# Performance work log

Measured on AMD Instinct MI355X. Metric: run time of the kernel, lower is better.

Reference implementation:

```python
import jax, jax.numpy as jnp
import numpy as np

# LLaMA-style decoder config (shrunken for reference): L layers, hidden D, H heads,
# SwiGLU width F, vocab V, LoRA rank R.
B, S, D, H, F, V, L, R = 2, 512, 1024, 16, 4096, 32000, 2, 16
DH = D // H
LORA_ALPHA = 32.0
EPS = 1e-5
ROPE_THETA = 10000.0


def setup_inputs() -> dict:
    key = jax.random.key(0)
    ks = iter(jax.random.split(key, 40))
    def n(shape, std=0.02):
        return jax.random.normal(next(ks), shape, jnp.float32) * std
    return {
        "input_ids": jax.random.randint(next(ks), (B, S), 0, V),
        "attention_mask": jnp.ones((B, S), jnp.int32),
        "embed": n((V, D)),
        "ln1": jnp.ones((L, D), jnp.float32),
        "ln2": jnp.ones((L, D), jnp.float32),
        "wq": n((L, D, D)), "aq": n((L, D, R)), "bq": n((L, R, D), 0.01),
        "wk": n((L, D, D)), "ak": n((L, D, R)), "bk": n((L, R, D), 0.01),
        "wv": n((L, D, D)), "av": n((L, D, R)), "bv": n((L, R, D), 0.01),
        "wo": n((L, D, D)), "ao": n((L, D, R)), "bo": n((L, R, D), 0.01),
        "wg": n((L, D, F)), "ag": n((L, D, R)), "bg": n((L, R, F), 0.01),
        "wu": n((L, D, F)), "au": n((L, D, R)), "bu": n((L, R, F), 0.01),
        "wd": n((L, F, D)), "ad": n((L, F, R)), "bd": n((L, R, D), 0.01),
        "final_ln": jnp.ones((D,), jnp.float32),
        "lm_head_w": n((D, V)),
        "value_w": n((D, 1)),
        "value_b": jnp.zeros((1,), jnp.float32),
    }


def _rmsnorm(x, w):
    return x * jax.lax.rsqrt(jnp.mean(x * x, axis=-1, keepdims=True) + EPS) * w


def _lin_lora(x, w, a, b):
    # base matmul + low-rank LoRA update scaled by alpha/r (dropout=eval/off)
    return x @ w + ((x @ a) @ b) * (LORA_ALPHA / R)


def _rope_cache(seq_len):
    half = DH // 2
    inv = 1.0 / (ROPE_THETA ** (jnp.arange(half, dtype=jnp.float32) / half))
    ang = jnp.arange(seq_len, dtype=jnp.float32)[:, None] * inv  # [S, half]
    ang = jnp.concatenate([ang, ang], axis=-1)                   # [S, DH]
    return jnp.cos(ang), jnp.sin(ang)


def _apply_rope(x, cos, sin):  # x: [B,S,H,DH]
    h = DH // 2
    rot = jnp.concatenate([-x[..., h:], x[..., :h]], axis=-1)
    return x * cos[None, :, None, :] + rot * sin[None, :, None, :]


def reference(input_ids, attention_mask, embed, ln1, ln2,
              wq, aq, bq, wk, ak, bk, wv, av, bv, wo, ao, bo,
              wg, ag, bg, wu, au, bu, wd, ad, bd,
              final_ln, lm_head_w, value_w, value_b):
    h = embed[input_ids]  # [B,S,D]
    cos, sin = _rope_cache(S)
    causal = jnp.tril(jnp.ones((S, S), bool))
    keep = causal[None, None, :, :] & (attention_mask[:, None, None, :] > 0)
    bias = jnp.where(keep, 0.0, -1e9)  # [B,1,S,S]
    scale = 1.0 / jnp.sqrt(jnp.float32(DH))

    for i in range(L):
        # --- self-attention block ---
        x = _rmsnorm(h, ln1[i])
        q = _lin_lora(x, wq[i], aq[i], bq[i]).reshape(B, S, H, DH)
        k = _lin_lora(x, wk[i], ak[i], bk[i]).reshape(B, S, H, DH)
        v = _lin_lora(x, wv[i], av[i], bv[i]).reshape(B, S, H, DH)
        q = _apply_rope(q, cos, sin)
        k = _apply_rope(k, cos, sin)
        scores = jnp.einsum("bqhd,bkhd->bhqk", q, k) * scale + bias
        attn = jax.nn.softmax(scores, axis=-1)
        o = jnp.einsum("bhqk,bkhd->bqhd", attn, v).reshape(B, S, D)
        h = h + _lin_lora(o, wo[i], ao[i], bo[i])
        # --- SwiGLU MLP block ---
        x = _rmsnorm(h, ln2[i])
        g = jax.nn.silu(_lin_lora(x, wg[i], ag[i], bg[i]))
        u = _lin_lora(x, wu[i], au[i], bu[i])
        h = h + _lin_lora(g * u, wd[i], ad[i], bd[i])

    h = _rmsnorm(h, final_ln)          # HF hidden_states[-1] is post final norm
    logits = h @ lm_head_w             # [B,S,V]
    values = (h @ value_w)[..., 0] + value_b[0]  # [B,S] (squeeze(-1))
    return logits, values
```

## Files before the change

kernel.cpp:

```cpp
#include <hip/hip_runtime.h>
#include <math.h>

constexpr int B = 2, S = 512, D = 1024, H = 16, F = 4096, V = 32000, L = 2, R = 16, DH = 64;
constexpr int BS = B * S;
constexpr float LORA_SCALE = 2.0f;
constexpr float EPS = 1e-5f;
constexpr int RS_QKV = 3 * D;
constexpr int RS_GU  = 2 * F;

typedef __attribute__((ext_vector_type(8))) __bf16 bf16x8;
typedef __attribute__((ext_vector_type(4))) float f32x4;

__device__ __forceinline__ unsigned short f2bf(float f) {
  unsigned u = __builtin_bit_cast(unsigned, f);
  unsigned r = (u + 0x7FFFu + ((u >> 16) & 1u)) >> 16;
  return (unsigned short)r;
}
__device__ __forceinline__ float bf2f(unsigned short us) {
  return __builtin_bit_cast(float, (unsigned)us << 16);
}
__device__ __forceinline__ void load_lds16(const void* g, void* l) {
  __builtin_amdgcn_global_load_lds((const __attribute__((address_space(1))) void*)g,
                                   (__attribute__((address_space(3))) void*)l, 16, 0, 0);
}

struct Ptr3 { const float* p[3]; };

__global__ void rope_cache_kernel(float* __restrict__ cosb, float* __restrict__ sinb) {
  int s = blockIdx.x, j = threadIdx.x;
  float inv = __expf(-(float)j * (9.210340371976184f / 32.0f));
  float ang = (float)s * inv;
  float c = cosf(ang), sn = sinf(ang);
  cosb[s * DH + j] = c;  cosb[s * DH + j + 32] = c;
  sinb[s * DH + j] = sn; sinb[s * DH + j + 32] = sn;
}

__global__ void embed_kernel(const int* __restrict__ ids, const float* __restrict__ emb,
                             float* __restrict__ h) {
  int row = blockIdx.x, t = threadIdx.x;
  int id = ids[row];
  ((float4*)(h + (size_t)row * D))[t] = ((const float4*)(emb + (size_t)id * D))[t];
}

__global__ void rmsnorm_bf16_kernel(const float* __restrict__ x, const float* __restrict__ w,
                                    unsigned short* __restrict__ y) {
  int row = blockIdx.x, t = threadIdx.x;
  float4 xv = ((const float4*)(x + (size_t)row * D))[t];
  float ss = xv.x * xv.x + xv.y * xv.y + xv.z * xv.z + xv.w * xv.w;
  __shared__ float red[256];
  red[t] = ss; __syncthreads();
  for (int s2 = 128; s2; s2 >>= 1) { if (t < s2) red[t] += red[t + s2]; __syncthreads(); }
  float rinv = rsqrtf(red[0] * (1.0f / D) + EPS);
  float4 wv = ((const float4*)w)[t];
  ushort4 o;
  o.x = f2bf(xv.x * rinv * wv.x); o.y = f2bf(xv.y * rinv * wv.y);
  o.z = f2bf(xv.z * rinv * wv.z); o.w = f2bf(xv.w * rinv * wv.w);
  ((ushort4*)(y + (size_t)row * D))[t] = o;
}

template <int NA>
__global__ void rms_lora_kernel(const float* __restrict__ hp, const float* __restrict__ w,
                                Ptr3 ap, unsigned short* __restrict__ xbf,
                                unsigned short* __restrict__ t2e) {
  int row = blockIdx.x, t = threadIdx.x;
  int lane = t & 63;
  __shared__ float xs[D];
  __shared__ float red[256];
  float4 xv = ((const float4*)(hp + (size_t)row * D))[t];
  float ss = xv.x * xv.x + xv.y * xv.y + xv.z * xv.z + xv.w * xv.w;
  red[t] = ss; __syncthreads();
  for (int s2 = 128; s2; s2 >>= 1) { if (t < s2) red[t] += red[t + s2]; __syncthreads(); }
  float rinv = rsqrtf(red[0] * (1.0f / D) + EPS);
  float4 wv = ((const float4*)w)[t];
  float4 nx;
  nx.x = xv.x * rinv * wv.x; nx.y = xv.y * rinv * wv.y;
  nx.z = xv.z * rinv * wv.z; nx.w = xv.w * rinv * wv.w;
  xs[t * 4 + 0] = nx.x; xs[t * 4 + 1] = nx.y; xs[t * 4 + 2] = nx.z; xs[t * 4 + 3] = nx.w;
  ushort4 o;
  o.x = f2bf(nx.x); o.y = f2bf(nx.y); o.z = f2bf(nx.z); o.w = f2bf(nx.w);
  ((ushort4*)(xbf + (size_t)row * D))[t] = o;
  if (t >= NA * 16 && t < 64) t2e[(size_t)row * 64 + t] = 0;
  __syncthreads();
  int n = t & 15, g = t >> 4;
#pragma unroll
  for (int ad = 0; ad < NA; ++ad) {
    const float* a = ap.p[ad];
    float s = 0.0f;
    for (int k = g; k < D; k += 16) s = fmaf(xs[k], a[k * 16 + n], s);
    s += __shfl_xor(s, 16);
    s += __shfl_xor(s, 32);
    if (lane < 16) red[(t >> 6) * 16 + n] = s;
    __syncthreads();
    if (t < 16) t2e[(size_t)row * 64 + ad * 16 + t] =
        f2bf(LORA_SCALE * (red[t] + red[t + 16] + red[t + 32] + red[t + 48]));
    if (ad + 1 < NA) __syncthreads();
  }
}

__global__ void lora_o_kernel(const unsigned short* __restrict__ xb, const float* __restrict__ a,
                              unsigned short* __restrict__ t2e) {
  int row = blockIdx.x, t = threadIdx.x;
  int lane = t & 63;
  __shared__ float xs[D];
  __shared__ float red[64];
  for (int k = t; k < D; k += 256) xs[k] = bf2f(xb[(size_t)row * D + k]);
  if (t >= 16 && t < 64) t2e[(size_t)row * 64 + t] = 0;
  __syncthreads();
  int n = t & 15, g = t >> 4;
  float s = 0.0f;
  for (int k = g; k < D; k += 16) s = fmaf(xs[k], a[k * 16 + n], s);
  s += __shfl_xor(s, 16);
  s += __shfl_xor(s, 32);
  if (lane < 16) red[(t >> 6) * 16 + n] = s;
  __syncthreads();
  if (t < 16) t2e[(size_t)row * 64 + t] =
      f2bf(LORA_SCALE * (red[t] + red[t + 16] + red[t + 32] + red[t + 48]));
}

__global__ void silu_lora_kernel(const unsigned short* __restrict__ gub, const float* __restrict__ a,
                                 unsigned short* __restrict__ gbf, unsigned short* __restrict__ t2e) {
  int row = blockIdx.x, t = threadIdx.x;
  int lane = t & 63;
  __shared__ float xs[F];
  __shared__ float red[64];
#pragma unroll
  for (int i2 = 0; i2 < 2; ++i2) {
    int idx = i2 * 256 + t;
    uint4 gv = ((const uint4*)(gub + (size_t)row * RS_GU))[idx];
    uint4 uv = ((const uint4*)(gub + (size_t)row * RS_GU + F))[idx];
    const unsigned* gw = (const unsigned*)&gv;
    const unsigned* uw = (const unsigned*)&uv;
    unsigned short go[8];
#pragma unroll
    for (int q = 0; q < 4; ++q) {
      float g0 = bf2f((unsigned short)(gw[q] & 0xffff)), g1 = bf2f((unsigned short)(gw[q] >> 16));
      float u0 = bf2f((unsigned short)(uw[q] & 0xffff)), u1 = bf2f((unsigned short)(uw[q] >> 16));
      float r0 = g0 / (1.0f + __expf(-g0)) * u0;
      float r1 = g1 / (1.0f + __expf(-g1)) * u1;
      xs[idx * 8 + q * 2] = r0; xs[idx * 8 + q * 2 + 1] = r1;
      go[q * 2] = f2bf(r0); go[q * 2 + 1] = f2bf(r1);
    }
    *(uint4*)(gbf + (size_t)row * F + idx * 8) = *(const uint4*)go;
  }
  if (t >= 16 && t < 64) t2e[(size_t)row * 64 + t] = 0;
  __syncthreads();
  int n = t & 15, g = t >> 4;
  float s = 0.0f;
  for (int k = g; k < F; k += 16) s = fmaf(xs[k], a[k * 16 + n], s);
  s += __shfl_xor(s, 16);
  s += __shfl_xor(s, 32);
  if (lane < 16) red[(t >> 6) * 16 + n] = s;
  __syncthreads();
  if (t < 16) t2e[(size_t)row * 64 + t] =
      f2bf(LORA_SCALE * (red[t] + red[t + 16] + red[t + 32] + red[t + 48]));
}

struct BD { const float* p0; const float* p1; const float* p2;
            unsigned short* dst; int NA; int logW; int nelem; };
struct BDs { BD d[8]; };
__global__ void bext_many_kernel(BDs da) {
  int gid = blockIdx.x * 256 + threadIdx.x;
  int di = 0;
  while (gid >= da.d[di].nelem) { gid -= da.d[di].nelem; ++di; }
  const BD dd = da.d[di];
  int n = gid >> 6, kk = gid & 63;
  int W = 1 << dd.logW;
  int sel = n >> dd.logW;
  const float* bp = (sel == 0) ? dd.p0 : (sel == 1) ? dd.p1 : dd.p2;
  float v = 0.0f;
  if ((kk >> 4) == sel && sel < dd.NA)
    v = bp[(size_t)(kk & 15) * W + (n & (W - 1))];
  dd.dst[(size_t)n * 64 + kk] = f2bf(v);
}

struct TD { const float* src; unsigned short* dst; int K; int N; int nblk; };
struct TDs { TD d[15]; };
__global__ __launch_bounds__(256) void transpose_many_kernel(TDs da) {
  __shared__ unsigned short tile[64 * 136];
  int bid = blockIdx.x;
  int di = 0;
  while (bid >= da.d[di].nblk) { bid -= da.d[di].nblk; ++di; }
  const TD dd = da.d[di];
  int nbx = dd.N >> 6;
  int n0 = (bid % nbx) * 64, k0 = (bid / nbx) * 128;
  int t = threadIdx.x;
  int rr = t >> 4, c4 = (t & 15) << 2;
#pragma unroll
  for (int i = 0; i < 8; ++i) {
    int row = i * 16 + rr;
    float4 v = *(const float4*)(dd.src + (size_t)(k0 + row) * dd.N + n0 + c4);
    tile[(c4 + 0) * 136 + (row ^ ((((c4 + 0) >> 2) & 7) << 2))] = f2bf(v.x);
    tile[(c4 + 1) * 136 + (row ^ ((((c4 + 1) >> 2) & 7) << 2))] = f2bf(v.y);
    tile[(c4 + 2) * 136 + (row ^ ((((c4 + 2) >> 2) & 7) << 2))] = f2bf(v.z);
    tile[(c4 + 3) * 136 + (row ^ ((((c4 + 3) >> 2) & 7) << 2))] = f2bf(v.w);
  }
  __syncthreads();
#pragma unroll
  for (int i = 0; i < 8; ++i) {
    int flat = i * 256 + t;
    int n = flat >> 5, cw = flat & 31;
    int kb = (cw * 4) ^ (((n >> 2) & 7) << 2);
    *(ushort4*)(dd.dst + (size_t)(n0 + n) * dd.K + k0 + cw * 4) =
        *(const ushort4*)(tile + n * 136 + kb);
  }
}

template <int BN, bool ACC, bool EXT, int OM>
__global__ __launch_bounds__(256) void gemm_bf16_kernel(
    const unsigned short* __restrict__ A, const unsigned short* __restrict__ Bt,
    void* __restrict__ Cp, int M, int N, int K,
    const unsigned short* __restrict__ Ae, const unsigned short* __restrict__ Be,
    const float* __restrict__ cosb, const float* __restrict__ sinb) {
  constexpr int WM = (BN == 128) ? 2 : 4;
  constexpr int RW = 128 / WM;
  constexpr int MI = RW / 16;
  constexpr int BCH = BN / 32;
  __shared__ __align__(16) unsigned short As[2][128 * 64];
  __shared__ __align__(16) unsigned short Bs[2][BN * 64];
  int t = threadIdx.x;
  int lane = t & 63, wave = t >> 6;
  int wr = (BN == 128) ? (wave >> 1) : wave;
  int wc = (BN == 128) ? (wave & 1) : 0;
  int MT = gridDim.y, NT = gridDim.x;
  int nwg = MT * NT;
  int orig = blockIdx.y * NT + blockIdx.x;
  int qq = nwg >> 3, rr8 = nwg & 7;
  int xcd = orig & 7, pos = orig >> 3;
  int wg = (xcd < rr8) ? (xcd * (qq + 1) + pos) : (rr8 * (qq + 1) + (xcd - rr8) * qq + pos);
  int m0 = (wg % MT) * 128, n0 = (wg / MT) * BN;
  int fr = lane & 15, fq = lane >> 4;
  int xorv = fr & 7;
  f32x4 acc[MI][4] = {};
  int kIters = K / 64;
  int nIters = EXT ? kIters + 1 : kIters;

  auto STAGE = [&](int it, int buf) {
    bool ext = EXT && (it == kIters);
    int k0 = it * 64;
#pragma unroll
    for (int c = 0; c < 4; ++c) {
      int i = c * 256 + t;
      int row = i >> 3, c8 = i & 7;
      int sc = (c8 ^ (row & 7)) * 8;
      const unsigned short* src = ext ? (Ae + (size_t)(m0 + row) * 64 + sc)
                                      : (A + (size_t)(m0 + row) * K + k0 + sc);
      load_lds16(src, &As[buf][i * 8]);
    }
#pragma unroll
    for (int c = 0; c < BCH; ++c) {
      int i = c * 256 + t;
      int row = i >> 3, c8 = i & 7;
      int sc = (c8 ^ (row & 7)) * 8;
      const unsigned short* src = ext ? (Be + (size_t)(n0 + row) * 64 + sc)
                                      : (Bt + (size_t)(n0 + row) * K + k0 + sc);
      load_lds16(src, &Bs[buf][i * 8]);
    }
  };

  STAGE(0, 0);
  if (nIters > 1) STAGE(1, 1);
  int cur = 0;
  for (int it = 0; it < nIters; ++it) {
    if (it + 1 < nIters) {
      if constexpr (BN == 128) asm volatile("s_waitcnt vmcnt(8)" ::: "memory");
      else                     asm volatile("s_waitcnt vmcnt(6)" ::: "memory");
    } else {
      asm volatile("s_waitcnt vmcnt(0)" ::: "memory");
    }
    __builtin_amdgcn_s_barrier();
    __builtin_amdgcn_s_setprio(1);
#pragma unroll
    for (int kk = 0; kk < 2; ++kk) {
      bf16x8 af[MI], bfr[4];
#pragma unroll
      for (int mi = 0; mi < MI; ++mi)
        af[mi] = *(const bf16x8*)(&As[cur][(wr * RW + mi * 16 + fr) * 64 + (((kk * 4 + fq) ^ xorv) << 3)]);
#pragma unroll
      for (int ni = 0; ni < 4; ++ni)
        bfr[ni] = *(const bf16x8*)(&Bs[cur][(wc * 64 + ni * 16 + fr) * 64 + (((kk * 4 + fq) ^ xorv) << 3)]);
#pragma unroll
      for (int mi = 0; mi < MI; ++mi)
#pragma unroll
        for (int ni = 0; ni < 4; ++ni)
          acc[mi][ni] = __builtin_amdgcn_mfma_f32_16x16x32_bf16(af[mi], bfr[ni], acc[mi][ni], 0, 0, 0);
    }
    __builtin_amdgcn_s_setprio(0);
    __builtin_amdgcn_s_barrier();
    if (it + 2 < nIters) STAGE(it + 2, cur);
    cur ^= 1;
  }
  if constexpr (OM == 0) {
    float* C = (float*)Cp;
#pragma unroll
    for (int mi = 0; mi < MI; ++mi)
#pragma unroll
      for (int ni = 0; ni < 4; ++ni)
#pragma unroll
        for (int j = 0; j < 4; ++j) {
          int r = m0 + wr * RW + mi * 16 + fq * 4 + j;
          int cl = n0 + wc * 64 + ni * 16 + fr;
          size_t idx = (size_t)r * N + cl;
          float v = acc[mi][ni][j];
          C[idx] = ACC ? C[idx] + v : v;
        }
  } else {
    unsigned short* Cb = (unsigned short*)Cp;
#pragma unroll
    for (int mi = 0; mi < MI; ++mi)
#pragma unroll
      for (int j = 0; j < 4; ++j) {
        int r = m0 + wr * RW + mi * 16 + fq * 4 + j;
        if constexpr (OM == 2) {
          int s = r & (S - 1);
#pragma unroll
          for (int ni = 0; ni < 2; ++ni) {
            int cl0 = n0 + wc * 64 + ni * 16 + fr;
            int cl1 = cl0 + 32;
            float x0 = acc[mi][ni][j], x1 = acc[mi][ni + 2][j];
            if (cl0 < 2 * D) {
              int dh = cl0 & 63;
              float cz = cosb[s * DH + dh], sz = sinb[s * DH + dh];
              float y0 = x0 * cz - x1 * sz;
              float y1 = x1 * cz + x0 * sz;
              x0 = y0; x1 = y1;
            }
            Cb[(size_t)r * N + cl0] = f2bf(x0);
            Cb[(size_t)r * N + cl1] = f2bf(x1);
          }
        } else {
#pragma unroll
          for (int ni = 0; ni < 4; ++ni) {
            int cl = n0 + wc * 64 + ni * 16 + fr;
            Cb[(size_t)r * N + cl] = f2bf(acc[mi][ni][j]);
          }
        }
      }
  }
}

__global__ __launch_bounds__(128) void attn_mfma_kernel(
    const unsigned short* __restrict__ qkvb, const int* __restrict__ amask,
    unsigned short* __restrict__ o) {
  __shared__ unsigned short Qs[32 * 72];
  __shared__ unsigned short Ks[64 * 72];
  __shared__ unsigned short Vt[64 * 72];
  __shared__ unsigned short Ps[2][16 * 72];
  __shared__ float msk[64];
  int bid = blockIdx.x;
  int qt = bid & 15, hh = (bid >> 4) & (H - 1), b = bid >> 8;
  int t = threadIdx.x;
  int lane = t & 63, w = t >> 6;
  int fr = lane & 15, fq = lane >> 4;
  size_t rowbase = (size_t)b * S;
  int q0 = qt * 32;
  const float scale = 0.125f;
#pragma unroll
  for (int c = 0; c < 2; ++c) {
    int i = c * 128 + t;
    int row = i >> 3, ch = i & 7;
    *(uint4*)(Qs + row * 72 + ch * 8) =
        *(const uint4*)(qkvb + (rowbase + q0 + row) * RS_QKV + hh * DH + ch * 8);
  }
  f32x4 oacc[4] = {};
  float m_old[4] = {-1e30f, -1e30f, -1e30f, -1e30f};
  float l[4] = {};
  int qbase = q0 + w * 16;
  int nkt = ((q0 + 31) >> 6) + 1;
  for (int kt = 0; kt < nkt; ++kt) {
    int kk0 = kt * 64;
#pragma unroll
    for (int c = 0; c < 4; ++c) {
      int i = c * 128 + t;
      int row = i >> 3, ch = i & 7;
      uint4 kv = *(const uint4*)(qkvb + (rowbase + kk0 + row) * RS_QKV + D + hh * DH + ch * 8);
      *(uint4*)(Ks + row * 72 + ch * 8) = kv;
      uint4 vv = *(const uint4*)(qkvb + (rowbase + kk0 + row) * RS_QKV + 2 * D + hh * DH + ch * 8);
      const unsigned short* vs = (const unsigned short*)&vv;
#pragma unroll
      for (int q = 0; q < 8; ++q) Vt[(ch * 8 + q) * 72 + row] = vs[q];
    }
    if (t < 64) msk[t] = (amask[b * S + kk0 + t] > 0) ? 0.0f : -1e9f;
    __syncthreads();
    bf16x8 aq[2];
    aq[0] = *(const bf16x8*)(Qs + (w * 16 + fr) * 72 + fq * 8);
    aq[1] = *(const bf16x8*)(Qs + (w * 16 + fr) * 72 + 32 + fq * 8);
    f32x4 sacc[4];
    __builtin_amdgcn_s_setprio(1);
#pragma unroll
    for (int ct = 0; ct < 4; ++ct) {
      bf16x8 bk0 = *(const bf16x8*)(Ks + (ct * 16 + fr) * 72 + fq * 8);
      bf16x8 bk1 = *(const bf16x8*)(Ks + (ct * 16 + fr) * 72 + 32 + fq * 8);
      f32x4 z = {};
      z = __builtin_amdgcn_mfma_f32_16x16x32_bf16(aq[0], bk0, z, 0, 0, 0);
      sacc[ct] = __builtin_amdgcn_mfma_f32_16x16x32_bf16(aq[1], bk1, z, 0, 0, 0);
    }
    __builtin_amdgcn_s_setprio(0);
    float sv[4][4];
#pragma unroll
    for (int ct = 0; ct < 4; ++ct) {
      int kg = kk0 + ct * 16 + fr;
      float mk = msk[ct * 16 + fr];
#pragma unroll
      for (int j = 0; j < 4; ++j) {
        int qg = qbase + fq * 4 + j;
        float s = sacc[ct][j] * scale + mk;
        sv[ct][j] = (kg > qg) ? -1e9f : s;
      }
    }
    float mnew[4], f[4], rsum[4];
#pragma unroll
    for (int j = 0; j < 4; ++j) {
      float mt = fmaxf(fmaxf(sv[0][j], sv[1][j]), fmaxf(sv[2][j], sv[3][j]));
      for (int off = 1; off < 16; off <<= 1) mt = fmaxf(mt, __shfl_xor(mt, off));
      mnew[j] = fmaxf(m_old[j], mt);
      f[j] = __expf(m_old[j] - mnew[j]);
      float rs = 0.0f;
#pragma unroll
      for (int ct = 0; ct < 4; ++ct) {
        float e = __expf(sv[ct][j] - mnew[j]);
        sv[ct][j] = e;
        rs += e;
      }
      for (int off = 1; off < 16; off <<= 1) rs += __shfl_xor(rs, off);
      rsum[j] = rs;
      l[j] = l[j] * f[j] + rsum[j];
      m_old[j] = mnew[j];
#pragma unroll
      for (int dt = 0; dt < 4; ++dt) oacc[dt][j] *= f[j];
    }
#pragma unroll
    for (int ct = 0; ct < 4; ++ct)
#pragma unroll
      for (int j = 0; j < 4; ++j)
        Ps[w][(fq * 4 + j) * 72 + ct * 16 + fr] = f2bf(sv[ct][j]);
    __syncthreads();
    bf16x8 pa[2];
    pa[0] = *(const bf16x8*)(&Ps[w][fr * 72 + fq * 8]);
    pa[1] = *(const bf16x8*)(&Ps[w][fr * 72 + 32 + fq * 8]);
    __builtin_amdgcn_s_setprio(1);
#pragma unroll
    for (int dt = 0; dt < 4; ++dt) {
      bf16x8 vb0 = *(const bf16x8*)(Vt + (dt * 16 + fr) * 72 + fq * 8);
      bf16x8 vb1 = *(const bf16x8*)(Vt + (dt * 16 + fr) * 72 + 32 + fq * 8);
      oacc[dt] = __builtin_amdgcn_mfma_f32_16x16x32_bf16(pa[0], vb0, oacc[dt], 0, 0, 0);
      oacc[dt] = __builtin_amdgcn_mfma_f32_16x16x32_bf16(pa[1], vb1, oacc[dt], 0, 0, 0);
    }
    __builtin_amdgcn_s_setprio(0);
    __syncthreads();
  }
#pragma unroll
  for (int j = 0; j < 4; ++j) {
    float rinv = 1.0f / l[j];
    int qrow = qbase + fq * 4 + j;
#pragma unroll
    for (int dt = 0; dt < 4; ++dt)
      o[(rowbase + qrow) * D + hh * DH + dt * 16 + fr] = f2bf(oacc[dt][j] * rinv);
  }
}

__global__ void value_kernel(const unsigned short* __restrict__ hf, const float* __restrict__ vw,
                             const float* __restrict__ vb, float* __restrict__ out) {
  int row = blockIdx.x, t = threadIdx.x;
  float acc = 0.0f;
  for (int d = t; d < D; d += 256) acc = fmaf(bf2f(hf[(size_t)row * D + d]), vw[d], acc);
  __shared__ float red[256];
  red[t] = acc; __syncthreads();
  for (int s2 = 128; s2; s2 >>= 1) { if (t < s2) red[t] += red[t + s2]; __syncthreads(); }
  if (t == 0) out[row] = red[0] + vb[0];
}

extern "C" void kernel_launch(void* const* d_in, const int* in_sizes, int n_in,
                              void* d_out, int out_size, void* d_ws, size_t ws_size,
                              hipStream_t stream) {
  const int*   ids     = (const int*)d_in[0];
  const int*   amask   = (const int*)d_in[1];
  const float* emb     = (const float*)d_in[2];
  const float* ln1     = (const float*)d_in[3];
  const float* ln2     = (const float*)d_in[4];
  const float* wq = (const float*)d_in[5],  *aq = (const float*)d_in[6],  *bq = (const float*)d_in[7];
  const float* wk = (const float*)d_in[8],  *ak = (const float*)d_in[9],  *bk = (const float*)d_in[10];
  const float* wv = (const float*)d_in[11], *av = (const float*)d_in[12], *bv = (const float*)d_in[13];
  const float* wo = (const float*)d_in[14], *ao = (const float*)d_in[15], *bo = (const float*)d_in[16];
  const float* wg = (const float*)d_in[17], *ag = (const float*)d_in[18], *bg = (const float*)d_in[19];
  const float* wu = (const float*)d_in[20], *au = (const float*)d_in[21], *bu = (const float*)d_in[22];
  const float* wd = (const float*)d_in[23], *ad = (const float*)d_in[24], *bd = (const float*)d_in[25];
  const float* final_ln  = (const float*)d_in[26];
  const float* lm_head_w = (const float*)d_in[27];
  const float* value_w   = (const float*)d_in[28];
  const float* value_b   = (const float*)d_in[29];

  float* out    = (float*)d_out;
  float* logits = out;
  float* values = out + (size_t)BS * V;

  float* Wf = (float*)d_ws;
  float* cosb = Wf; Wf += S * DH;
  float* sinb = Wf; Wf += S * DH;
  float* h    = Wf; Wf += (size_t)BS * D;
  unsigned short* Wb = (unsigned short*)Wf;
  unsigned short* x_bf  = Wb; Wb += (size_t)BS * D;
  unsigned short* t2e   = Wb; Wb += (size_t)BS * 64;
  unsigned short* qg    = Wb; Wb += (size_t)BS * F;
  unsigned short* gu_bf = Wb; Wb += (size_t)BS * RS_GU;
  unsigned short* wqkvT = Wb; Wb += (size_t)L * 3 * D * D;
  unsigned short* woT   = Wb; Wb += (size_t)L * D * D;
  unsigned short* wguT  = Wb; Wb += (size_t)L * 2 * D * F;
  unsigned short* wdT   = Wb; Wb += (size_t)L * F * D;
  unsigned short* lmT   = Wb; Wb += (size_t)D * V;
  unsigned short* beQKV = Wb; Wb += (size_t)L * 3 * D * 64;
  unsigned short* beO   = Wb; Wb += (size_t)L * D * 64;
  unsigned short* beGU  = Wb; Wb += (size_t)L * 2 * F * 64;
  unsigned short* beD   = Wb; Wb += (size_t)L * D * 64;
  unsigned short* qkv_bf = qg;
  unsigned short* gbf    = qg;
  unsigned short* obf    = gu_bf;

  TDs td; int tblocks = 0; int di = 0;
  auto addT = [&](const float* s, unsigned short* dp, int K_, int N_) {
    td.d[di] = {s, dp, K_, N_, (K_ / 128) * (N_ / 64)};
    tblocks += td.d[di].nblk; ++di;
  };
  for (int l = 0; l < L; ++l) {
    size_t DD = (size_t)D * D, DF = (size_t)D * F;
    addT(wq + l * DD, wqkvT + (size_t)l * 3 * DD, D, D);
    addT(wk + l * DD, wqkvT + (size_t)l * 3 * DD + DD, D, D);
    addT(wv + l * DD, wqkvT + (size_t)l * 3 * DD + 2 * DD, D, D);
    addT(wo + l * DD, woT + l * DD, D, D);
    addT(wg + l * DF, wguT + (size_t)l * 2 * DF, D, F);
    addT(wu + l * DF, wguT + (size_t)l * 2 * DF + DF, D, F);
    addT(wd + l * DF, wdT + l * DF, F, D);
  }
  addT(lm_head_w, lmT, D, V);
  transpose_many_kernel<<<dim3(tblocks), 256, 0, stream>>>(td);

  BDs bd2; int belems = 0; di = 0;
  auto addB = [&](const float* p0, const float* p1, const float* p2,
                  unsigned short* dst, int NA, int logW, int N_) {
    bd2.d[di] = {p0, p1, p2, dst, NA, logW, N_ * 64};
    belems += N_ * 64; ++di;
  };
  for (int l = 0; l < L; ++l) {
    size_t oRD = (size_t)l * R * D, oRF = (size_t)l * R * F;
    addB(bq + oRD, bk + oRD, bv + oRD, beQKV + (size_t)l * 3 * D * 64, 3, 10, 3 * D);
    addB(bo + oRD, nullptr, nullptr,   beO   + (size_t)l * D * 64,     1, 10, D);
    addB(bg + oRF, bu + oRF, nullptr,  beGU  + (size_t)l * 2 * F * 64, 2, 12, 2 * F);
    addB(bd + oRD, nullptr, nullptr,   beD   + (size_t)l * D * 64,     1, 10, D);
  }
  bext_many_kernel<<<dim3(belems / 256), 256, 0, stream>>>(bd2);

  rope_cache_kernel<<<dim3(S), dim3(32), 0, stream>>>(cosb, sinb);
  embed_kernel<<<dim3(BS), dim3(256), 0, stream>>>(ids, emb, h);

  for (int l = 0; l < L; ++l) {
    size_t DD = (size_t)D * D, DF = (size_t)D * F;
    size_t oDR = (size_t)l * D * R, oFR = (size_t)l * F * R;

    { Ptr3 ap = {{aq + oDR, ak + oDR, av + oDR}};
      rms_lora_kernel<3><<<dim3(BS), 256, 0, stream>>>(h, ln1 + (size_t)l * D, ap, x_bf, t2e); }
    gemm_bf16_kernel<128, false, true, 2><<<dim3(3 * D / 128, BS / 128), 256, 0, stream>>>(
        x_bf, wqkvT + (size_t)l * 3 * DD, qkv_bf, BS, 3 * D, D,
        t2e, beQKV + (size_t)l * 3 * D * 64, cosb, sinb);

    attn_mfma_kernel<<<dim3(B * H * (S / 32)), 128, 0, stream>>>(qkv_bf, amask, obf);

    lora_o_kernel<<<dim3(BS), 256, 0, stream>>>(obf, ao + oDR, t2e);
    gemm_bf16_kernel<64, true, true, 0><<<dim3(D / 64, BS / 128), 256, 0, stream>>>(
        obf, woT + l * DD, h, BS, D, D, t2e, beO + (size_t)l * D * 64, nullptr, nullptr);

    { Ptr3 ap = {{ag + oDR, au + oDR, nullptr}};
      rms_lora_kernel<2><<<dim3(BS), 256, 0, stream>>>(h, ln2 + (size_t)l * D, ap, x_bf, t2e); }
    gemm_bf16_kernel<128, false, true, 1><<<dim3(2 * F / 128, BS / 128), 256, 0, stream>>>(
        x_bf, wguT + (size_t)l * 2 * DF, gu_bf, BS, 2 * F, D,
        t2e, beGU + (size_t)l * 2 * F * 64, nullptr, nullptr);

    silu_lora_kernel<<<dim3(BS), 256, 0, stream>>>(gu_bf, ad + oFR, gbf, t2e);

    gemm_bf16_kernel<64, true, true, 0><<<dim3(D / 64, BS / 128), 256, 0, stream>>>(
        gbf, wdT + l * DF, h, BS, D, F, t2e, beD + (size_t)l * D * 64, nullptr, nullptr);
  }

  rmsnorm_bf16_kernel<<<dim3(BS), 256, 0, stream>>>(h, final_ln, x_bf);
  gemm_bf16_kernel<128, false, false, 0><<<dim3(V / 128, BS / 128), 256, 0, stream>>>(
      x_bf, lmT, logits, BS, V, D, nullptr, nullptr, nullptr, nullptr);
  value_kernel<<<dim3(BS), 256, 0, stream>>>(x_bf, value_w, value_b, values);
}
```

Before: 1.045 ms.

## Add 256x256 LM-head GEMM, widen attention query tiles, drop setprio hints

Adds a dedicated 512-thread GEMM with 256x256 tiles and XCD-aware workgroup remapping, used for the large vocabulary projection. It aims to raise operand reuse and L2 locality over the generic 128-wide tile kernel. Attention now handles 64 query rows per block with four waves, so each K/V tile loaded into shared memory serves more queries and the causal loop bound becomes simpler. All s_setprio hints are removed from the GEMM and attention kernels. The costs are heavy LDS use (128 KB) and high register pressure in the new GEMM, which limit occupancy, plus fewer attention blocks.

```diff
diff --git a/kernel.cpp b/kernel.cpp
--- a/kernel.cpp
+++ b/kernel.cpp
@@ -268,7 +268,6 @@
       asm volatile("s_waitcnt vmcnt(0)" ::: "memory");
     }
     __builtin_amdgcn_s_barrier();
-    __builtin_amdgcn_s_setprio(1);
 #pragma unroll
     for (int kk = 0; kk < 2; ++kk) {
       bf16x8 af[MI], bfr[4];
@@ -284,7 +283,6 @@
         for (int ni = 0; ni < 4; ++ni)
           acc[mi][ni] = __builtin_amdgcn_mfma_f32_16x16x32_bf16(af[mi], bfr[ni], acc[mi][ni], 0, 0, 0);
     }
-    __builtin_amdgcn_s_setprio(0);
     __builtin_amdgcn_s_barrier();
     if (it + 2 < nIters) STAGE(it + 2, cur);
     cur ^= 1;
@@ -338,25 +336,101 @@
   }
 }
 
-__global__ __launch_bounds__(128) void attn_mfma_kernel(
+__global__ __launch_bounds__(512) void gemm256_kernel(
+    const unsigned short* __restrict__ A, const unsigned short* __restrict__ Bt,
+    float* __restrict__ C, int M, int N, int K) {
+  __shared__ __align__(16) unsigned short As[2][256 * 64];
+  __shared__ __align__(16) unsigned short Bs[2][256 * 64];
+  int t = threadIdx.x;
+  int lane = t & 63, wave = t >> 6;
+  int wr = wave >> 2, wc = wave & 3;
+  int MT = gridDim.y, NT = gridDim.x;
+  int nwg = MT * NT;
+  int orig = blockIdx.y * NT + blockIdx.x;
+  int qq = nwg >> 3, rr8 = nwg & 7;
+  int xcd = orig & 7, pos = orig >> 3;
+  int wg = (xcd < rr8) ? (xcd * (qq + 1) + pos) : (rr8 * (qq + 1) + (xcd - rr8) * qq + pos);
+  int m0 = (wg % MT) * 256, n0 = (wg / MT) * 256;
+  int fr = lane & 15, fq = lane >> 4;
+  int xorv = fr & 7;
+  f32x4 acc[8][4] = {};
+  int kIters = K / 64;
+
+  auto STAGE = [&](int it, int buf) {
+    int k0 = it * 64;
+#pragma unroll
+    for (int c = 0; c < 4; ++c) {
+      int i = c * 512 + t;
+      int row = i >> 3, c8 = i & 7;
+      int sc = (c8 ^ (row & 7)) * 8;
+      load_lds16(A + (size_t)(m0 + row) * K + k0 + sc, &As[buf][i * 8]);
+    }
+#pragma unroll
+    for (int c = 0; c < 4; ++c) {
+      int i = c * 512 + t;
+      int row = i >> 3, c8 = i & 7;
+      int sc = (c8 ^ (row & 7)) * 8;
+      load_lds16(Bt + (size_t)(n0 + row) * K + k0 + sc, &Bs[buf][i * 8]);
+    }
+  };
+
+  STAGE(0, 0);
+  if (kIters > 1) STAGE(1, 1);
+  int cur = 0;
+  for (int it = 0; it < kIters; ++it) {
+    if (it + 1 < kIters) asm volatile("s_waitcnt vmcnt(8)" ::: "memory");
+    else                 asm volatile("s_waitcnt vmcnt(0)" ::: "memory");
+    __builtin_amdgcn_s_barrier();
+#pragma unroll
+    for (int kk = 0; kk < 2; ++kk) {
+      bf16x8 af[8], bfr[4];
+#pragma unroll
+      for (int mi = 0; mi < 8; ++mi)
+        af[mi] = *(const bf16x8*)(&As[cur][(wr * 128 + mi * 16 + fr) * 64 + (((kk * 4 + fq) ^ xorv) << 3)]);
+#pragma unroll
+      for (int ni = 0; ni < 4; ++ni)
+        bfr[ni] = *(const bf16x8*)(&Bs[cur][(wc * 64 + ni * 16 + fr) * 64 + (((kk * 4 + fq) ^ xorv) << 3)]);
+#pragma unroll
+      for (int mi = 0; mi < 8; ++mi)
+#pragma unroll
+        for (int ni = 0; ni < 4; ++ni)
+          acc[mi][ni] = __builtin_amdgcn_mfma_f32_16x16x32_bf16(af[mi], bfr[ni], acc[mi][ni], 0, 0, 0);
+    }
+    __builtin_amdgcn_s_barrier();
+    if (it + 2 < kIters) STAGE(it + 2, cur);
+    cur ^= 1;
+  }
+#pragma unroll
+  for (int mi = 0; mi < 8; ++mi)
+#pragma unroll
+    for (int ni = 0; ni < 4; ++ni)
+#pragma unroll
+      for (int j = 0; j < 4; ++j) {
+        int r = m0 + wr * 128 + mi * 16 + fq * 4 + j;
+        int cl = n0 + wc * 64 + ni * 16 + fr;
+        C[(size_t)r * N + cl] = acc[mi][ni][j];
+      }
+}
+
+__global__ __launch_bounds__(256) void attn_mfma_kernel(
     const unsigned short* __restrict__ qkvb, const int* __restrict__ amask,
     unsigned short* __restrict__ o) {
-  __shared__ unsigned short Qs[32 * 72];
+  __shared__ unsigned short Qs[64 * 72];
   __shared__ unsigned short Ks[64 * 72];
   __shared__ unsigned short Vt[64 * 72];
-  __shared__ unsigned short Ps[2][16 * 72];
+  __shared__ unsigned short Ps[4][16 * 72];
   __shared__ float msk[64];
   int bid = blockIdx.x;
-  int qt = bid & 15, hh = (bid >> 4) & (H - 1), b = bid >> 8;
+  int qt = bid & 7, hh = (bid >> 3) & (H - 1), b = bid >> 7;
   int t = threadIdx.x;
   int lane = t & 63, w = t >> 6;
   int fr = lane & 15, fq = lane >> 4;
   size_t rowbase = (size_t)b * S;
-  int q0 = qt * 32;
+  int q0 = qt * 64;
   const float scale = 0.125f;
 #pragma unroll
   for (int c = 0; c < 2; ++c) {
-    int i = c * 128 + t;
+    int i = c * 256 + t;
     int row = i >> 3, ch = i & 7;
     *(uint4*)(Qs + row * 72 + ch * 8) =
         *(const uint4*)(qkvb + (rowbase + q0 + row) * RS_QKV + hh * DH + ch * 8);
@@ -365,12 +439,11 @@
   float m_old[4] = {-1e30f, -1e30f, -1e30f, -1e30f};
   float l[4] = {};
   int qbase = q0 + w * 16;
-  int nkt = ((q0 + 31) >> 6) + 1;
-  for (int kt = 0; kt < nkt; ++kt) {
+  for (int kt = 0; kt <= qt; ++kt) {
     int kk0 = kt * 64;
 #pragma unroll
-    for (int c = 0; c < 4; ++c) {
-      int i = c * 128 + t;
+    for (int c = 0; c < 2; ++c) {
+      int i = c * 256 + t;
       int row = i >> 3, ch = i & 7;
       uint4 kv = *(const uint4*)(qkvb + (rowbase + kk0 + row) * RS_QKV + D + hh * DH + ch * 8);
       *(uint4*)(Ks + row * 72 + ch * 8) = kv;
@@ -385,7 +458,6 @@
     aq[0] = *(const bf16x8*)(Qs + (w * 16 + fr) * 72 + fq * 8);
     aq[1] = *(const bf16x8*)(Qs + (w * 16 + fr) * 72 + 32 + fq * 8);
     f32x4 sacc[4];
-    __builtin_amdgcn_s_setprio(1);
 #pragma unroll
     for (int ct = 0; ct < 4; ++ct) {
       bf16x8 bk0 = *(const bf16x8*)(Ks + (ct * 16 + fr) * 72 + fq * 8);
@@ -394,7 +466,6 @@
       z = __builtin_amdgcn_mfma_f32_16x16x32_bf16(aq[0], bk0, z, 0, 0, 0);
       sacc[ct] = __builtin_amdgcn_mfma_f32_16x16x32_bf16(aq[1], bk1, z, 0, 0, 0);
     }
-    __builtin_amdgcn_s_setprio(0);
     float sv[4][4];
 #pragma unroll
     for (int ct = 0; ct < 4; ++ct) {
@@ -437,7 +508,6 @@
     bf16x8 pa[2];
     pa[0] = *(const bf16x8*)(&Ps[w][fr * 72 + fq * 8]);
     pa[1] = *(const bf16x8*)(&Ps[w][fr * 72 + 32 + fq * 8]);
-    __builtin_amdgcn_s_setprio(1);
 #pragma unroll
     for (int dt = 0; dt < 4; ++dt) {
       bf16x8 vb0 = *(const bf16x8*)(Vt + (dt * 16 + fr) * 72 + fq * 8);
@@ -445,7 +515,6 @@
       oacc[dt] = __builtin_amdgcn_mfma_f32_16x16x32_bf16(pa[0], vb0, oacc[dt], 0, 0, 0);
       oacc[dt] = __builtin_amdgcn_mfma_f32_16x16x32_bf16(pa[1], vb1, oacc[dt], 0, 0, 0);
     }
-    __builtin_amdgcn_s_setprio(0);
     __syncthreads();
   }
 #pragma unroll
@@ -561,7 +630,7 @@
         x_bf, wqkvT + (size_t)l * 3 * DD, qkv_bf, BS, 3 * D, D,
         t2e, beQKV + (size_t)l * 3 * D * 64, cosb, sinb);
 
-    attn_mfma_kernel<<<dim3(B * H * (S / 32)), 128, 0, stream>>>(qkv_bf, amask, obf);
+    attn_mfma_kernel<<<dim3(B * H * (S / 64)), 256, 0, stream>>>(qkv_bf, amask, obf);
 
     lora_o_kernel<<<dim3(BS), 256, 0, stream>>>(obf, ao + oDR, t2e);
     gemm_bf16_kernel<64, true, true, 0><<<dim3(D / 64, BS / 128), 256, 0, stream>>>(
@@ -580,7 +649,6 @@
   }
 
   rmsnorm_bf16_kernel<<<dim3(BS), 256, 0, stream>>>(h, final_ln, x_bf);
-  gemm_bf16_kernel<128, false, false, 0><<<dim3(V / 128, BS / 128), 256, 0, stream>>>(
-      x_bf, lmT, logits, BS, V, D, nullptr, nullptr, nullptr, nullptr);
+  gemm256_kernel<<<dim3(V / 256, BS / 256), 512, 0, stream>>>(x_bf, lmT, logits, BS, V, D);
   value_kernel<<<dim3(BS), 256, 0, stream>>>(x_bf, value_w, value_b, values);
 }
```

After: 1.007 ms. 1.04x faster.
